# Kernel tuning notes

Hardware: AMD Instinct MI355X
Metric: run time of the kernel (lower is better)

Reference implementation:

```python
import jax, jax.numpy as jnp
import numpy as np

DIVERSITY_WEIGHT = 0.3
UNCERTAINTY_WEIGHT = 0.3
EPS_NORM = 1e-12  # torch F.normalize eps
EPS_LOG = 1e-8


def setup_inputs() -> dict:
    key = jax.random.key(0)
    k1, k2 = jax.random.split(key)
    B, N, D, C = 8, 8192, 512, 2
    x = jax.random.normal(k1, (B, N, D), dtype=jnp.float32)
    c = jax.random.normal(k2, (B, N, C), dtype=jnp.float32)
    return {"x": x, "c": c, "big_lambda": 512}


def reference(x, c, big_lambda):
    B, N, D = x.shape
    C = c.shape[-1]
    big_lambda = min(big_lambda, N)

    # relevance: max class score per instance (C > 1 branch)
    if C == 1:
        relevance = c[..., 0]
    else:
        relevance = jnp.max(c, axis=-1)  # [B, N]

    # diversity: 1 - mean cosine similarity to all other patches.
    # Row-sum of the N x N cosine-sim matrix factorizes:
    #   sum_j xn_i . xn_j = xn_i . (sum_j xn_j)  -> O(N*D) instead of O(N^2*D)
    norms = jnp.linalg.norm(x, axis=-1, keepdims=True)
    x_norm = x / jnp.maximum(norms, EPS_NORM)          # [B, N, D]
    s = jnp.sum(x_norm, axis=1)                        # [B, D]
    row_sums = jnp.einsum('bnd,bd->bn', x_norm, s)     # [B, N]
    avg_sim = (row_sums - 1.0) / (N - 1)
    diversity = 1.0 - avg_sim

    # uncertainty: entropy of class distribution
    if C == 1:
        p = jax.nn.sigmoid(c[..., 0])
        probs = jnp.stack([1.0 - p, p], axis=-1)
    else:
        probs = jax.nn.softmax(c, axis=-1)
    uncertainty = -jnp.sum(probs * jnp.log(probs + EPS_LOG), axis=-1)  # [B, N]

    combined = relevance + DIVERSITY_WEIGHT * diversity + UNCERTAINTY_WEIGHT * uncertainty

    _, selected_indices = jax.lax.top_k(combined, big_lambda)  # [B, big_lambda]
    attention_weights = jax.nn.softmax(combined, axis=1)       # [B, N]
    return selected_indices, attention_weights
```

## Files before the change

kernel.cpp:

```cpp
#include <hip/hip_runtime.h>
#include <stdint.h>

#define B 8
#define N 8192
#define D 512
#define K 512
#define DIV_W 0.3f
#define UNC_W 0.3f

constexpr int ROWS_PER_WAVE  = 16;
constexpr int WAVES_PER_BLK  = 4;
constexpr int ROWS_PER_BLOCK = ROWS_PER_WAVE * WAVES_PER_BLK;
constexpr int BLOCKS_PER_B   = N / ROWS_PER_BLOCK;

constexpr float DIVC = DIV_W * (1.0f + 1.0f / 8191.0f);
constexpr float COEF = DIV_W / 8191.0f;

__device__ __forceinline__ uint32_t ordmap(float f) {
    uint32_t u = __float_as_uint(f);
    return (u & 0x80000000u) ? ~u : (u | 0x80000000u);
}
__device__ __forceinline__ float ordunmap(uint32_t u) {
    return (u >> 31) ? __uint_as_float(u & 0x7FFFFFFFu) : __uint_as_float(~u);
}

__global__ __launch_bounds__(256) void k_norm_s(const float* __restrict__ x,
                                                const float* __restrict__ c,
                                                float* __restrict__ inv_norm,
                                                float* __restrict__ partials,
                                                float* __restrict__ combined) {
    int blk  = blockIdx.x;
    int b    = blk / BLOCKS_PER_B;
    int rb   = (blk % BLOCKS_PER_B) * ROWS_PER_BLOCK;
    int tid  = threadIdx.x;
    int wave = tid >> 6;
    int lane = tid & 63;

    const float4* xb = (const float4*)(x + (size_t)b * N * D);

    float4 accA = {0.f, 0.f, 0.f, 0.f};
    float4 accB = {0.f, 0.f, 0.f, 0.f};

    int row0 = rb + wave * ROWS_PER_WAVE;
    for (int r = 0; r < ROWS_PER_WAVE; ++r) {
        int row = row0 + r;
        const float4* xr = xb + (size_t)row * (D / 4);
        float4 a  = xr[lane];
        float4 bb = xr[64 + lane];

        float ss = a.x*a.x + a.y*a.y + a.z*a.z + a.w*a.w
                 + bb.x*bb.x + bb.y*bb.y + bb.z*bb.z + bb.w*bb.w;
        #pragma unroll
        for (int o = 32; o > 0; o >>= 1) ss += __shfl_xor(ss, o, 64);

        float inv = 1.0f / fmaxf(sqrtf(ss), 1e-12f);
        if (lane == 0) inv_norm[b * N + row] = inv;

        accA.x += a.x * inv;  accA.y += a.y * inv;
        accA.z += a.z * inv;  accA.w += a.w * inv;
        accB.x += bb.x * inv; accB.y += bb.y * inv;
        accB.z += bb.z * inv; accB.w += bb.w * inv;
    }

    if (lane < 16) {
        int row = row0 + lane;
        float2 cv = ((const float2*)(c))[(size_t)b * N + row];
        float rel = fmaxf(cv.x, cv.y);
        float e0 = expf(cv.x - rel), e1 = expf(cv.y - rel);
        float Z  = e0 + e1;
        float p0 = e0 / Z, p1 = e1 / Z;
        float ent = -(p0 * logf(p0 + 1e-8f) + p1 * logf(p1 + 1e-8f));
        combined[b * N + row] = rel + UNC_W * ent + DIVC;
    }

    __shared__ float sp[WAVES_PER_BLK][D];
    float* dA = &sp[wave][lane * 4];
    dA[0] = accA.x; dA[1] = accA.y; dA[2] = accA.z; dA[3] = accA.w;
    float* dB = &sp[wave][256 + lane * 4];
    dB[0] = accB.x; dB[1] = accB.y; dB[2] = accB.z; dB[3] = accB.w;
    __syncthreads();

    float* dst = partials + (size_t)blk * D;
    for (int d = tid; d < D; d += 256)
        dst[d] = sp[0][d] + sp[1][d] + sp[2][d] + sp[3][d];
}

__global__ __launch_bounds__(512) void k_reduce_s(const float* __restrict__ partials,
                                                  float* __restrict__ s) {
    int b = blockIdx.x;
    int d = threadIdx.x;
    const float* p = partials + (size_t)b * BLOCKS_PER_B * D + d;
    float acc = 0.f;
    #pragma unroll 16
    for (int j = 0; j < BLOCKS_PER_B; ++j) acc += p[(size_t)j * D];
    s[b * D + d] = acc;
}

__global__ __launch_bounds__(256) void k_combined(const float* __restrict__ x,
                                                  const float* __restrict__ inv_norm,
                                                  const float* __restrict__ s,
                                                  float* __restrict__ combined) {
    __shared__ float sl[D];
    int blk  = blockIdx.x;
    int b    = blk / BLOCKS_PER_B;
    int rb   = (blk % BLOCKS_PER_B) * ROWS_PER_BLOCK;
    int tid  = threadIdx.x;
    int wave = tid >> 6;
    int lane = tid & 63;

    for (int d = tid; d < D; d += 256) sl[d] = s[b * D + d];
    __syncthreads();

    const float4* sv = (const float4*)sl;
    float4 sA = sv[lane];
    float4 sB = sv[64 + lane];

    const float4* xb = (const float4*)(x + (size_t)b * N * D);
    int row0 = rb + wave * ROWS_PER_WAVE;
    for (int r = 0; r < ROWS_PER_WAVE; ++r) {
        int row = row0 + r;
        const float4* xr = xb + (size_t)row * (D / 4);
        float4 a  = xr[lane];
        float4 bb = xr[64 + lane];

        float dot = a.x*sA.x + a.y*sA.y + a.z*sA.z + a.w*sA.w
                  + bb.x*sB.x + bb.y*sB.y + bb.z*sB.z + bb.w*sB.w;
        #pragma unroll
        for (int o = 32; o > 0; o >>= 1) dot += __shfl_xor(dot, o, 64);

        if (lane == 0) {
            float rs = dot * inv_norm[b * N + row];
            combined[b * N + row] = combined[b * N + row] - COEF * rs;
        }
    }
}

__global__ __launch_bounds__(1024) void k_topk_sm(const float* __restrict__ combined,
                                                  float* __restrict__ out_idx,
                                                  float* __restrict__ out_w) {
    __shared__ uint64_t cand[K];
    __shared__ uint32_t hist[256];
    __shared__ uint32_t tiew[256];
    __shared__ uint32_t wred[16];
    __shared__ float    fred[16];
    __shared__ uint32_t sc_prefix, sc_remK, sc_cnt;

    const int b    = blockIdx.x;
    const int tid  = threadIdx.x;
    const int lane = tid & 63;
    const int wave = tid >> 6;

    const float4* cb4 = (const float4*)(combined + b * N);
    float4 f0 = cb4[tid];
    float4 f1 = cb4[1024 + tid];

    uint32_t v[8];
    v[0] = ordmap(f0.x); v[1] = ordmap(f0.y); v[2] = ordmap(f0.z); v[3] = ordmap(f0.w);
    v[4] = ordmap(f1.x); v[5] = ordmap(f1.y); v[6] = ordmap(f1.z); v[7] = ordmap(f1.w);

    uint32_t umax = 0;
    #pragma unroll
    for (int q = 0; q < 8; ++q) umax = max(umax, v[q]);
    #pragma unroll
    for (int o = 32; o > 0; o >>= 1) umax = max(umax, __shfl_xor(umax, o, 64));
    if (lane == 0) wred[wave] = umax;
    if (tid == 0) { sc_remK = K; sc_prefix = 0u; sc_cnt = 0u; }
    __syncthreads();
    uint32_t bmax = wred[0];
    #pragma unroll
    for (int q = 1; q < 16; ++q) bmax = max(bmax, wred[q]);
    const float m = ordunmap(bmax);

    float e[8];
    float sum = 0.f;
    #pragma unroll
    for (int q = 0; q < 8; ++q) { e[q] = expf(ordunmap(v[q]) - m); sum += e[q]; }
    #pragma unroll
    for (int o = 32; o > 0; o >>= 1) sum += __shfl_xor(sum, o, 64);
    if (lane == 0) fred[wave] = sum;
    __syncthreads();
    float Z = 0.f;
    #pragma unroll
    for (int q = 0; q < 16; ++q) Z += fred[q];
    const float invZ = 1.0f / Z;
    float4* ow = (float4*)(out_w + b * N);
    float4 w0 = {e[0]*invZ, e[1]*invZ, e[2]*invZ, e[3]*invZ};
    float4 w1 = {e[4]*invZ, e[5]*invZ, e[6]*invZ, e[7]*invZ};
    ow[tid]        = w0;
    ow[1024 + tid] = w1;

    uint32_t prefix = 0, maskHi = 0;
    for (int p = 3; p >= 0; --p) {
        if (tid < 256) hist[tid] = 0u;
        __syncthreads();
        const int sh = 8 * p;
        if (p == 3) {
            #pragma unroll
            for (int q = 0; q < 8; ++q) {
                uint32_t bin = v[q] >> 24;
                bool pred = true;
                unsigned long long todo = ~0ULL;
                while (todo) {
                    int leader = __ffsll(todo) - 1;
                    uint32_t lbin = __shfl(bin, leader, 64);
                    unsigned long long same = __ballot(pred && (bin == lbin));
                    if (lane == leader) atomicAdd(&hist[lbin], (uint32_t)__popcll(same));
                    todo &= ~same;
                    if (bin == lbin) pred = false;
                }
            }
        } else {
            #pragma unroll
            for (int q = 0; q < 8; ++q) {
                if ((v[q] & maskHi) == prefix)
                    atomicAdd(&hist[(v[q] >> sh) & 0xFFu], 1u);
            }
        }
        __syncthreads();
        if (wave == 0) {
            uint32_t cc[4], lsum = 0;
            #pragma unroll
            for (int q = 0; q < 4; ++q) { cc[q] = hist[lane * 4 + q]; lsum += cc[q]; }
            uint32_t ssum = lsum;
            #pragma unroll
            for (int off = 1; off < 64; off <<= 1) {
                uint32_t t2 = __shfl_down(ssum, off, 64);
                if (lane + off < 64) ssum += t2;
            }
            uint32_t cum = ssum - lsum;
            const uint32_t remK = sc_remK;
            #pragma unroll
            for (int q = 3; q >= 0; --q) {
                if (cum < remK && cum + cc[q] >= remK) {
                    sc_prefix = prefix | ((uint32_t)(lane * 4 + q) << sh);
                    sc_remK   = remK - cum;
                }
                cum += cc[q];
            }
        }
        __syncthreads();
        prefix = sc_prefix;
        maskHi |= (0xFFu << sh);
    }
    const uint32_t T    = prefix;
    const uint32_t remF = sc_remK;

    if (tid < 256) tiew[tid] = 0u;
    __syncthreads();
    #pragma unroll
    for (int q = 0; q < 8; ++q) {
        uint32_t idx = (q < 4) ? (uint32_t)(4 * tid + q)
                               : (uint32_t)(4096 + 4 * tid + (q - 4));
        bool g = (v[q] > T);
        unsigned long long mask = __ballot(g);
        if (mask) {
            int leader = __ffsll(mask) - 1;
            uint32_t bcnt = (uint32_t)__popcll(mask);
            uint32_t wbase = 0;
            if (lane == leader) wbase = atomicAdd(&sc_cnt, bcnt);
            wbase = __shfl(wbase, leader, 64);
            if (g) {
                uint32_t off = (uint32_t)__popcll(mask & ((1ULL << lane) - 1ULL));
                cand[wbase + off] = ((uint64_t)v[q] << 13) | (uint32_t)(8191 - idx);
            }
        }
        if (v[q] == T) atomicOr(&tiew[idx >> 5], 1u << (idx & 31));
    }
    __syncthreads();
    const uint32_t base = sc_cnt;
    if (wave == 0) {
        const int w0i = lane * 4;
        uint32_t lsum = 0;
        #pragma unroll
        for (int q = 0; q < 4; ++q) lsum += __popc(tiew[w0i + q]);
        uint32_t ssum = lsum;
        #pragma unroll
        for (int off = 1; off < 64; off <<= 1) {
            uint32_t t2 = __shfl_up(ssum, off, 64);
            if (lane >= off) ssum += t2;
        }
        uint32_t rank = ssum - lsum;
        for (int q = 0; q < 4; ++q) {
            uint32_t word = tiew[w0i + q];
            while (word) {
                int bpos = __builtin_ctz(word);
                if (rank < remF) {
                    uint32_t idx = (uint32_t)(w0i + q) * 32u + (uint32_t)bpos;
                    cand[base + rank] = ((uint64_t)T << 13) | (uint32_t)(8191 - idx);
                }
                rank++;
                word &= word - 1;
            }
        }
    }
    __syncthreads();

    uint64_t sv = (tid < K) ? cand[tid] : 0ULL;
    __syncthreads();
    for (int k = 2; k <= K; k <<= 1) {
        for (int j = k >> 1; j > 0; j >>= 1) {
            const bool desc  = ((tid & k) == 0);
            const bool lower = ((tid & j) == 0);
            uint64_t pv;
            if (j >= 64) {
                if (tid < K) cand[tid] = sv;
                __syncthreads();
                pv = (tid < K) ? cand[tid ^ j] : 0ULL;
                __syncthreads();
            } else {
                pv = __shfl_xor(sv, j, 64);
            }
            const bool keepmax = (lower == desc);
            if (tid < K && (keepmax ? (pv > sv) : (pv < sv))) sv = pv;
        }
    }
    if (tid < K)
        out_idx[b * K + tid] = (float)(8191u - (uint32_t)(sv & 0x1FFFu));
}

extern "C" void kernel_launch(void* const* d_in, const int* in_sizes, int n_in,
                              void* d_out, int out_size, void* d_ws, size_t ws_size,
                              hipStream_t stream) {
    const float* x = (const float*)d_in[0];
    const float* c = (const float*)d_in[1];

    float* ws       = (float*)d_ws;
    float* partials = ws;
    float* s        = partials + B * BLOCKS_PER_B * D;
    float* inv_norm = s + B * D;
    float* combined = inv_norm + B * N;

    float* out = (float*)d_out;

    k_norm_s  <<<B * BLOCKS_PER_B, 256, 0, stream>>>(x, c, inv_norm, partials, combined);
    k_reduce_s<<<B, 512, 0, stream>>>(partials, s);
    k_combined<<<B * BLOCKS_PER_B, 256, 0, stream>>>(x, inv_norm, s, combined);
    k_topk_sm <<<B, 1024, 0, stream>>>(combined, out, out + B * K);
}
```

Baseline: 81.14 us.

## Fuse all stages into one persistent kernel with software grid barriers

Replaces the four kernel launches with a single persistent kernel of 256 blocks × 512 threads that runs the norm and partial-sum pass, the per-batch reduction, the dot-product pass and the top-k/softmax pass, separated by atomic-based grid barriers. It also enlarges the per-block work from 64 to 256 rows and has the top-k stage use 512 threads holding 16 values each. The aim is to remove launch gaps and per-kernel ramp-up. The cost is barrier spin latency, a hipMemsetAsync on every call, and a reliance on all 256 blocks being co-resident, which can deadlock if they are not. Only 8 blocks do the reduction and top-k work while the rest sit idle.

New measurement: 172.3 us. +112.3%, slower.

```diff
diff --git a/kernel.cpp b/kernel.cpp
--- a/kernel.cpp
+++ b/kernel.cpp
@@ -8,10 +8,11 @@
 #define DIV_W 0.3f
 #define UNC_W 0.3f
 
-constexpr int ROWS_PER_WAVE  = 16;
-constexpr int WAVES_PER_BLK  = 4;
-constexpr int ROWS_PER_BLOCK = ROWS_PER_WAVE * WAVES_PER_BLK;
-constexpr int BLOCKS_PER_B   = N / ROWS_PER_BLOCK;
+constexpr int GRID    = 256;
+constexpr int THREADS = 512;
+constexpr int WAVES   = 8;
+constexpr int BLOCKS_PER_BATCH = 32;
+constexpr int ROWS_PER_BLOCK   = 256;
 
 constexpr float DIVC = DIV_W * (1.0f + 1.0f / 8191.0f);
 constexpr float COEF = DIV_W / 8191.0f;
@@ -24,298 +25,314 @@
     return (u >> 31) ? __uint_as_float(u & 0x7FFFFFFFu) : __uint_as_float(~u);
 }
 
-__global__ __launch_bounds__(256) void k_norm_s(const float* __restrict__ x,
-                                                const float* __restrict__ c,
-                                                float* __restrict__ inv_norm,
-                                                float* __restrict__ partials,
-                                                float* __restrict__ combined) {
-    int blk  = blockIdx.x;
-    int b    = blk / BLOCKS_PER_B;
-    int rb   = (blk % BLOCKS_PER_B) * ROWS_PER_BLOCK;
-    int tid  = threadIdx.x;
-    int wave = tid >> 6;
-    int lane = tid & 63;
-
+__device__ __forceinline__ void grid_barrier(unsigned int* bar) {
+    __syncthreads();
+    if (threadIdx.x == 0) {
+        __threadfence();
+        unsigned int g = atomicAdd(&bar[1], 0u);
+        __threadfence();
+        unsigned int prev = atomicAdd(&bar[0], 1u);
+        if (prev == GRID - 1) {
+            atomicExch(&bar[0], 0u);
+            __threadfence();
+            atomicAdd(&bar[1], 1u);
+        } else {
+            while (atomicAdd(&bar[1], 0u) == g)
+                __builtin_amdgcn_s_sleep(8);
+        }
+        __threadfence();
+    }
+    __syncthreads();
+}
+
+struct P3 {
+    unsigned long long cand[K];
+    uint32_t hist[256];
+    uint32_t tiew[256];
+    uint32_t wred[WAVES];
+    float    fred[WAVES];
+    uint32_t sc_prefix, sc_remK, sc_cnt;
+};
+
+__global__ __launch_bounds__(THREADS, 2) void k_fused(
+    const float* __restrict__ x, const float* __restrict__ c,
+    float* __restrict__ inv_norm, float* __restrict__ partials,
+    float* __restrict__ s, float* __restrict__ combined,
+    float* __restrict__ out_idx, float* __restrict__ out_w,
+    unsigned int* __restrict__ bar)
+{
+    __shared__ __align__(16) unsigned char smem[WAVES * D * 4];
+    float (*sp)[D] = (float(*)[D])smem;
+
+    const int bid  = blockIdx.x;
+    const int tid  = threadIdx.x;
+    const int wave = tid >> 6;
+    const int lane = tid & 63;
+
+    const int b     = bid >> 5;
+    const int rbase = (bid & 31) * ROWS_PER_BLOCK;
     const float4* xb = (const float4*)(x + (size_t)b * N * D);
 
-    float4 accA = {0.f, 0.f, 0.f, 0.f};
-    float4 accB = {0.f, 0.f, 0.f, 0.f};
-
-    int row0 = rb + wave * ROWS_PER_WAVE;
-    for (int r = 0; r < ROWS_PER_WAVE; ++r) {
-        int row = row0 + r;
-        const float4* xr = xb + (size_t)row * (D / 4);
-        float4 a  = xr[lane];
-        float4 bb = xr[64 + lane];
-
-        float ss = a.x*a.x + a.y*a.y + a.z*a.z + a.w*a.w
-                 + bb.x*bb.x + bb.y*bb.y + bb.z*bb.z + bb.w*bb.w;
-        #pragma unroll
-        for (int o = 32; o > 0; o >>= 1) ss += __shfl_xor(ss, o, 64);
-
-        float inv = 1.0f / fmaxf(sqrtf(ss), 1e-12f);
-        if (lane == 0) inv_norm[b * N + row] = inv;
-
-        accA.x += a.x * inv;  accA.y += a.y * inv;
-        accA.z += a.z * inv;  accA.w += a.w * inv;
-        accB.x += bb.x * inv; accB.y += bb.y * inv;
-        accB.z += bb.z * inv; accB.w += bb.w * inv;
-    }
-
-    if (lane < 16) {
-        int row = row0 + lane;
-        float2 cv = ((const float2*)(c))[(size_t)b * N + row];
-        float rel = fmaxf(cv.x, cv.y);
-        float e0 = expf(cv.x - rel), e1 = expf(cv.y - rel);
-        float Z  = e0 + e1;
-        float p0 = e0 / Z, p1 = e1 / Z;
-        float ent = -(p0 * logf(p0 + 1e-8f) + p1 * logf(p1 + 1e-8f));
-        combined[b * N + row] = rel + UNC_W * ent + DIVC;
-    }
-
-    __shared__ float sp[WAVES_PER_BLK][D];
-    float* dA = &sp[wave][lane * 4];
-    dA[0] = accA.x; dA[1] = accA.y; dA[2] = accA.z; dA[3] = accA.w;
-    float* dB = &sp[wave][256 + lane * 4];
-    dB[0] = accB.x; dB[1] = accB.y; dB[2] = accB.z; dB[3] = accB.w;
-    __syncthreads();
-
-    float* dst = partials + (size_t)blk * D;
-    for (int d = tid; d < D; d += 256)
-        dst[d] = sp[0][d] + sp[1][d] + sp[2][d] + sp[3][d];
-}
-
-__global__ __launch_bounds__(512) void k_reduce_s(const float* __restrict__ partials,
-                                                  float* __restrict__ s) {
-    int b = blockIdx.x;
-    int d = threadIdx.x;
-    const float* p = partials + (size_t)b * BLOCKS_PER_B * D + d;
-    float acc = 0.f;
-    #pragma unroll 16
-    for (int j = 0; j < BLOCKS_PER_B; ++j) acc += p[(size_t)j * D];
-    s[b * D + d] = acc;
-}
-
-__global__ __launch_bounds__(256) void k_combined(const float* __restrict__ x,
-                                                  const float* __restrict__ inv_norm,
-                                                  const float* __restrict__ s,
-                                                  float* __restrict__ combined) {
-    __shared__ float sl[D];
-    int blk  = blockIdx.x;
-    int b    = blk / BLOCKS_PER_B;
-    int rb   = (blk % BLOCKS_PER_B) * ROWS_PER_BLOCK;
-    int tid  = threadIdx.x;
-    int wave = tid >> 6;
-    int lane = tid & 63;
-
-    for (int d = tid; d < D; d += 256) sl[d] = s[b * D + d];
-    __syncthreads();
-
-    const float4* sv = (const float4*)sl;
-    float4 sA = sv[lane];
-    float4 sB = sv[64 + lane];
-
-    const float4* xb = (const float4*)(x + (size_t)b * N * D);
-    int row0 = rb + wave * ROWS_PER_WAVE;
-    for (int r = 0; r < ROWS_PER_WAVE; ++r) {
-        int row = row0 + r;
-        const float4* xr = xb + (size_t)row * (D / 4);
-        float4 a  = xr[lane];
-        float4 bb = xr[64 + lane];
-
-        float dot = a.x*sA.x + a.y*sA.y + a.z*sA.z + a.w*sA.w
-                  + bb.x*sB.x + bb.y*sB.y + bb.z*sB.z + bb.w*sB.w;
-        #pragma unroll
-        for (int o = 32; o > 0; o >>= 1) dot += __shfl_xor(dot, o, 64);
-
-        if (lane == 0) {
-            float rs = dot * inv_norm[b * N + row];
-            combined[b * N + row] = combined[b * N + row] - COEF * rs;
-        }
-    }
-}
-
-__global__ __launch_bounds__(1024) void k_topk_sm(const float* __restrict__ combined,
-                                                  float* __restrict__ out_idx,
-                                                  float* __restrict__ out_w) {
-    __shared__ uint64_t cand[K];
-    __shared__ uint32_t hist[256];
-    __shared__ uint32_t tiew[256];
-    __shared__ uint32_t wred[16];
-    __shared__ float    fred[16];
-    __shared__ uint32_t sc_prefix, sc_remK, sc_cnt;
-
-    const int b    = blockIdx.x;
-    const int tid  = threadIdx.x;
-    const int lane = tid & 63;
-    const int wave = tid >> 6;
-
-    const float4* cb4 = (const float4*)(combined + b * N);
-    float4 f0 = cb4[tid];
-    float4 f1 = cb4[1024 + tid];
-
-    uint32_t v[8];
-    v[0] = ordmap(f0.x); v[1] = ordmap(f0.y); v[2] = ordmap(f0.z); v[3] = ordmap(f0.w);
-    v[4] = ordmap(f1.x); v[5] = ordmap(f1.y); v[6] = ordmap(f1.z); v[7] = ordmap(f1.w);
-
-    uint32_t umax = 0;
-    #pragma unroll
-    for (int q = 0; q < 8; ++q) umax = max(umax, v[q]);
-    #pragma unroll
-    for (int o = 32; o > 0; o >>= 1) umax = max(umax, __shfl_xor(umax, o, 64));
-    if (lane == 0) wred[wave] = umax;
-    if (tid == 0) { sc_remK = K; sc_prefix = 0u; sc_cnt = 0u; }
-    __syncthreads();
-    uint32_t bmax = wred[0];
-    #pragma unroll
-    for (int q = 1; q < 16; ++q) bmax = max(bmax, wred[q]);
-    const float m = ordunmap(bmax);
-
-    float e[8];
-    float sum = 0.f;
-    #pragma unroll
-    for (int q = 0; q < 8; ++q) { e[q] = expf(ordunmap(v[q]) - m); sum += e[q]; }
-    #pragma unroll
-    for (int o = 32; o > 0; o >>= 1) sum += __shfl_xor(sum, o, 64);
-    if (lane == 0) fred[wave] = sum;
-    __syncthreads();
-    float Z = 0.f;
-    #pragma unroll
-    for (int q = 0; q < 16; ++q) Z += fred[q];
-    const float invZ = 1.0f / Z;
-    float4* ow = (float4*)(out_w + b * N);
-    float4 w0 = {e[0]*invZ, e[1]*invZ, e[2]*invZ, e[3]*invZ};
-    float4 w1 = {e[4]*invZ, e[5]*invZ, e[6]*invZ, e[7]*invZ};
-    ow[tid]        = w0;
-    ow[1024 + tid] = w1;
-
-    uint32_t prefix = 0, maskHi = 0;
-    for (int p = 3; p >= 0; --p) {
-        if (tid < 256) hist[tid] = 0u;
-        __syncthreads();
-        const int sh = 8 * p;
-        if (p == 3) {
+    {
+        float4 accA = {0.f,0.f,0.f,0.f}, accB = {0.f,0.f,0.f,0.f};
+        #pragma unroll
+        for (int chunk = 0; chunk < 2; ++chunk) {
+            const int row0 = rbase + chunk * 128 + wave * 16;
+            #pragma unroll 4
+            for (int r = 0; r < 16; ++r) {
+                const int row = row0 + r;
+                const float4* xr = xb + (size_t)row * (D / 4);
+                float4 a  = xr[lane];
+                float4 bb = xr[64 + lane];
+
+                float ss = a.x*a.x + a.y*a.y + a.z*a.z + a.w*a.w
+                         + bb.x*bb.x + bb.y*bb.y + bb.z*bb.z + bb.w*bb.w;
+                #pragma unroll
+                for (int o = 32; o > 0; o >>= 1) ss += __shfl_xor(ss, o, 64);
+
+                float inv = 1.0f / fmaxf(sqrtf(ss), 1e-12f);
+                if (lane == 0) inv_norm[b * N + row] = inv;
+
+                accA.x += a.x * inv;  accA.y += a.y * inv;
+                accA.z += a.z * inv;  accA.w += a.w * inv;
+                accB.x += bb.x * inv; accB.y += bb.y * inv;
+                accB.z += bb.z * inv; accB.w += bb.w * inv;
+            }
+            if (lane < 16) {
+                const int row = row0 + lane;
+                float2 cv = ((const float2*)c)[(size_t)b * N + row];
+                float rel = fmaxf(cv.x, cv.y);
+                float e0 = expf(cv.x - rel), e1 = expf(cv.y - rel);
+                float Z  = e0 + e1;
+                float p0 = e0 / Z, p1 = e1 / Z;
+                float ent = -(p0 * logf(p0 + 1e-8f) + p1 * logf(p1 + 1e-8f));
+                combined[b * N + row] = rel + UNC_W * ent + DIVC;
+            }
+        }
+
+        float* dA = &sp[wave][lane * 4];
+        dA[0] = accA.x; dA[1] = accA.y; dA[2] = accA.z; dA[3] = accA.w;
+        float* dB = &sp[wave][256 + lane * 4];
+        dB[0] = accB.x; dB[1] = accB.y; dB[2] = accB.z; dB[3] = accB.w;
+        __syncthreads();
+
+        float v = 0.f;
+        #pragma unroll
+        for (int w = 0; w < WAVES; ++w) v += sp[w][tid];
+        partials[(size_t)bid * D + tid] = v;
+    }
+    grid_barrier(bar);
+
+    if (bid < B) {
+        const float* p = partials + (size_t)bid * BLOCKS_PER_BATCH * D + tid;
+        float acc = 0.f;
+        #pragma unroll 8
+        for (int j = 0; j < BLOCKS_PER_BATCH; ++j) acc += p[(size_t)j * D];
+        s[bid * D + tid] = acc;
+    }
+    grid_barrier(bar);
+
+    {
+        float* sl = (float*)smem;
+        sl[tid] = s[b * D + tid];
+        __syncthreads();
+        float4 sA = ((const float4*)sl)[lane];
+        float4 sB = ((const float4*)sl)[64 + lane];
+
+        #pragma unroll
+        for (int chunk = 0; chunk < 2; ++chunk) {
+            const int row0 = rbase + chunk * 128 + wave * 16;
+            #pragma unroll 4
+            for (int r = 0; r < 16; ++r) {
+                const int row = row0 + r;
+                const float4* xr = xb + (size_t)row * (D / 4);
+                float4 a  = xr[lane];
+                float4 bb = xr[64 + lane];
+
+                float dot = a.x*sA.x + a.y*sA.y + a.z*sA.z + a.w*sA.w
+                          + bb.x*sB.x + bb.y*sB.y + bb.z*sB.z + bb.w*sB.w;
+                #pragma unroll
+                for (int o = 32; o > 0; o >>= 1) dot += __shfl_xor(dot, o, 64);
+
+                if (lane == 0) {
+                    float rs = dot * inv_norm[b * N + row];
+                    combined[b * N + row] -= COEF * rs;
+                }
+            }
+        }
+    }
+    grid_barrier(bar);
+
+    if (bid >= B) return;
+    {
+        P3* p3 = (P3*)smem;
+        const int bb3 = bid;
+        const float4* cb4 = (const float4*)(combined + bb3 * N);
+
+        uint32_t v[16];
+        uint32_t umax = 0;
+        #pragma unroll
+        for (int g = 0; g < 4; ++g) {
+            float4 f = cb4[tid + 512 * g];
+            v[4*g+0] = ordmap(f.x); v[4*g+1] = ordmap(f.y);
+            v[4*g+2] = ordmap(f.z); v[4*g+3] = ordmap(f.w);
+            umax = max(umax, max(max(v[4*g+0], v[4*g+1]), max(v[4*g+2], v[4*g+3])));
+        }
+        #pragma unroll
+        for (int o = 32; o > 0; o >>= 1) umax = max(umax, __shfl_xor(umax, o, 64));
+        if (lane == 0) p3->wred[wave] = umax;
+        if (tid == 0) { p3->sc_remK = K; p3->sc_prefix = 0u; p3->sc_cnt = 0u; }
+        __syncthreads();
+        uint32_t bmax = p3->wred[0];
+        #pragma unroll
+        for (int q = 1; q < WAVES; ++q) bmax = max(bmax, p3->wred[q]);
+        const float m = ordunmap(bmax);
+
+        float e[16];
+        float sum = 0.f;
+        #pragma unroll
+        for (int q = 0; q < 16; ++q) { e[q] = expf(ordunmap(v[q]) - m); sum += e[q]; }
+        #pragma unroll
+        for (int o = 32; o > 0; o >>= 1) sum += __shfl_xor(sum, o, 64);
+        if (lane == 0) p3->fred[wave] = sum;
+        __syncthreads();
+        float Z = 0.f;
+        #pragma unroll
+        for (int q = 0; q < WAVES; ++q) Z += p3->fred[q];
+        const float invZ = 1.0f / Z;
+        float4* ow = (float4*)(out_w + bb3 * N);
+        #pragma unroll
+        for (int g = 0; g < 4; ++g) {
+            float4 w = {e[4*g+0]*invZ, e[4*g+1]*invZ, e[4*g+2]*invZ, e[4*g+3]*invZ};
+            ow[tid + 512 * g] = w;
+        }
+
+        uint32_t prefix = 0, maskHi = 0;
+        for (int p = 3; p >= 0; --p) {
+            if (tid < 256) p3->hist[tid] = 0u;
+            __syncthreads();
+            const int sh = 8 * p;
+            if (p == 3) {
+                #pragma unroll
+                for (int q = 0; q < 16; ++q) {
+                    uint32_t bin = v[q] >> 24;
+                    bool pred = true;
+                    unsigned long long todo = ~0ULL;
+                    while (todo) {
+                        int leader = __ffsll(todo) - 1;
+                        uint32_t lbin = __shfl(bin, leader, 64);
+                        unsigned long long same = __ballot(pred && (bin == lbin));
+                        if (lane == leader) atomicAdd(&p3->hist[lbin], (uint32_t)__popcll(same));
+                        todo &= ~same;
+                        if (bin == lbin) pred = false;
+                    }
+                }
+            } else {
+                #pragma unroll
+                for (int q = 0; q < 16; ++q) {
+                    if ((v[q] & maskHi) == prefix)
+                        atomicAdd(&p3->hist[(v[q] >> sh) & 0xFFu], 1u);
+                }
+            }
+            __syncthreads();
+            if (wave == 0) {
+                uint32_t cc[4], lsum = 0;
+                #pragma unroll
+                for (int q = 0; q < 4; ++q) { cc[q] = p3->hist[lane * 4 + q]; lsum += cc[q]; }
+                uint32_t ssum = lsum;
+                #pragma unroll
+                for (int off = 1; off < 64; off <<= 1) {
+                    uint32_t t2 = __shfl_down(ssum, off, 64);
+                    if (lane + off < 64) ssum += t2;
+                }
+                uint32_t cum = ssum - lsum;
+                const uint32_t remK = p3->sc_remK;
+                #pragma unroll
+                for (int q = 3; q >= 0; --q) {
+                    if (cum < remK && cum + cc[q] >= remK) {
+                        p3->sc_prefix = prefix | ((uint32_t)(lane * 4 + q) << sh);
+                        p3->sc_remK   = remK - cum;
+                    }
+                    cum += cc[q];
+                }
+            }
+            __syncthreads();
+            prefix = p3->sc_prefix;
+            maskHi |= (0xFFu << sh);
+        }
+        const uint32_t T    = prefix;
+        const uint32_t remF = p3->sc_remK;
+
+        if (tid < 256) p3->tiew[tid] = 0u;
+        __syncthreads();
+        #pragma unroll
+        for (int q = 0; q < 16; ++q) {
+            uint32_t idx = 4u * tid + 2048u * (q >> 2) + (q & 3);
+            bool g = (v[q] > T);
+            unsigned long long mask = __ballot(g);
+            if (mask) {
+                int leader = __ffsll(mask) - 1;
+                uint32_t bcnt = (uint32_t)__popcll(mask);
+                uint32_t wbase = 0;
+                if (lane == leader) wbase = atomicAdd(&p3->sc_cnt, bcnt);
+                wbase = __shfl(wbase, leader, 64);
+                if (g) {
+                    uint32_t off = (uint32_t)__popcll(mask & ((1ULL << lane) - 1ULL));
+                    p3->cand[wbase + off] = ((uint64_t)v[q] << 13) | (uint32_t)(8191 - idx);
+                }
+            }
+            if (v[q] == T) atomicOr(&p3->tiew[idx >> 5], 1u << (idx & 31));
+        }
+        __syncthreads();
+        const uint32_t base = p3->sc_cnt;
+        if (wave == 0) {
+            const int w0i = lane * 4;
+            uint32_t lsum = 0;
             #pragma unroll
-            for (int q = 0; q < 8; ++q) {
-                uint32_t bin = v[q] >> 24;
-                bool pred = true;
-                unsigned long long todo = ~0ULL;
-                while (todo) {
-                    int leader = __ffsll(todo) - 1;
-                    uint32_t lbin = __shfl(bin, leader, 64);
-                    unsigned long long same = __ballot(pred && (bin == lbin));
-                    if (lane == leader) atomicAdd(&hist[lbin], (uint32_t)__popcll(same));
-                    todo &= ~same;
-                    if (bin == lbin) pred = false;
-                }
-            }
-        } else {
-            #pragma unroll
-            for (int q = 0; q < 8; ++q) {
-                if ((v[q] & maskHi) == prefix)
-                    atomicAdd(&hist[(v[q] >> sh) & 0xFFu], 1u);
-            }
-        }
-        __syncthreads();
-        if (wave == 0) {
-            uint32_t cc[4], lsum = 0;
-            #pragma unroll
-            for (int q = 0; q < 4; ++q) { cc[q] = hist[lane * 4 + q]; lsum += cc[q]; }
+            for (int q = 0; q < 4; ++q) lsum += __popc(p3->tiew[w0i + q]);
             uint32_t ssum = lsum;
             #pragma unroll
             for (int off = 1; off < 64; off <<= 1) {
-                uint32_t t2 = __shfl_down(ssum, off, 64);
-                if (lane + off < 64) ssum += t2;
-            }
-            uint32_t cum = ssum - lsum;
-            const uint32_t remK = sc_remK;
-            #pragma unroll
-            for (int q = 3; q >= 0; --q) {
-                if (cum < remK && cum + cc[q] >= remK) {
-                    sc_prefix = prefix | ((uint32_t)(lane * 4 + q) << sh);
-                    sc_remK   = remK - cum;
-                }
-                cum += cc[q];
-            }
-        }
-        __syncthreads();
-        prefix = sc_prefix;
-        maskHi |= (0xFFu << sh);
-    }
-    const uint32_t T    = prefix;
-    const uint32_t remF = sc_remK;
-
-    if (tid < 256) tiew[tid] = 0u;
-    __syncthreads();
-    #pragma unroll
-    for (int q = 0; q < 8; ++q) {
-        uint32_t idx = (q < 4) ? (uint32_t)(4 * tid + q)
-                               : (uint32_t)(4096 + 4 * tid + (q - 4));
-        bool g = (v[q] > T);
-        unsigned long long mask = __ballot(g);
-        if (mask) {
-            int leader = __ffsll(mask) - 1;
-            uint32_t bcnt = (uint32_t)__popcll(mask);
-            uint32_t wbase = 0;
-            if (lane == leader) wbase = atomicAdd(&sc_cnt, bcnt);
-            wbase = __shfl(wbase, leader, 64);
-            if (g) {
-                uint32_t off = (uint32_t)__popcll(mask & ((1ULL << lane) - 1ULL));
-                cand[wbase + off] = ((uint64_t)v[q] << 13) | (uint32_t)(8191 - idx);
-            }
-        }
-        if (v[q] == T) atomicOr(&tiew[idx >> 5], 1u << (idx & 31));
-    }
-    __syncthreads();
-    const uint32_t base = sc_cnt;
-    if (wave == 0) {
-        const int w0i = lane * 4;
-        uint32_t lsum = 0;
-        #pragma unroll
-        for (int q = 0; q < 4; ++q) lsum += __popc(tiew[w0i + q]);
-        uint32_t ssum = lsum;
-        #pragma unroll
-        for (int off = 1; off < 64; off <<= 1) {
-            uint32_t t2 = __shfl_up(ssum, off, 64);
-            if (lane >= off) ssum += t2;
-        }
-        uint32_t rank = ssum - lsum;
-        for (int q = 0; q < 4; ++q) {
-            uint32_t word = tiew[w0i + q];
-            while (word) {
-                int bpos = __builtin_ctz(word);
-                if (rank < remF) {
-                    uint32_t idx = (uint32_t)(w0i + q) * 32u + (uint32_t)bpos;
-                    cand[base + rank] = ((uint64_t)T << 13) | (uint32_t)(8191 - idx);
-                }
-                rank++;
-                word &= word - 1;
-            }
-        }
-    }
-    __syncthreads();
-
-    uint64_t sv = (tid < K) ? cand[tid] : 0ULL;
-    __syncthreads();
-    for (int k = 2; k <= K; k <<= 1) {
-        for (int j = k >> 1; j > 0; j >>= 1) {
-            const bool desc  = ((tid & k) == 0);
-            const bool lower = ((tid & j) == 0);
-            uint64_t pv;
-            if (j >= 64) {
-                if (tid < K) cand[tid] = sv;
-                __syncthreads();
-                pv = (tid < K) ? cand[tid ^ j] : 0ULL;
-                __syncthreads();
-            } else {
-                pv = __shfl_xor(sv, j, 64);
-            }
-            const bool keepmax = (lower == desc);
-            if (tid < K && (keepmax ? (pv > sv) : (pv < sv))) sv = pv;
-        }
-    }
-    if (tid < K)
-        out_idx[b * K + tid] = (float)(8191u - (uint32_t)(sv & 0x1FFFu));
+                uint32_t t2 = __shfl_up(ssum, off, 64);
+                if (lane >= off) ssum += t2;
+            }
+            uint32_t rank = ssum - lsum;
+            for (int q = 0; q < 4; ++q) {
+                uint32_t word = p3->tiew[w0i + q];
+                while (word) {
+                    int bpos = __builtin_ctz(word);
+                    if (rank < remF) {
+                        uint32_t idx = (uint32_t)(w0i + q) * 32u + (uint32_t)bpos;
+                        p3->cand[base + rank] = ((uint64_t)T << 13) | (uint32_t)(8191 - idx);
+                    }
+                    rank++;
+                    word &= word - 1;
+                }
+            }
+        }
+        __syncthreads();
+
+        uint64_t sv = p3->cand[tid];
+        __syncthreads();
+        for (int k = 2; k <= K; k <<= 1) {
+            for (int j = k >> 1; j > 0; j >>= 1) {
+                const bool desc  = ((tid & k) == 0);
+                const bool lower = ((tid & j) == 0);
+                uint64_t pv;
+                if (j >= 64) {
+                    p3->cand[tid] = sv;
+                    __syncthreads();
+                    pv = p3->cand[tid ^ j];
+                    __syncthreads();
+                } else {
+                    pv = __shfl_xor(sv, j, 64);
+                }
+                const bool keepmax = (lower == desc);
+                if (keepmax ? (pv > sv) : (pv < sv)) sv = pv;
+            }
+        }
+        out_idx[bb3 * K + tid] = (float)(8191u - (uint32_t)(sv & 0x1FFFu));
+    }
 }
 
 extern "C" void kernel_launch(void* const* d_in, const int* in_sizes, int n_in,
@@ -324,16 +341,17 @@
     const float* x = (const float*)d_in[0];
     const float* c = (const float*)d_in[1];
 
-    float* ws       = (float*)d_ws;
-    float* partials = ws;
-    float* s        = partials + B * BLOCKS_PER_B * D;
+    unsigned int* bar = (unsigned int*)d_ws;
+    float* base     = (float*)d_ws + 16;
+    float* partials = base;
+    float* s        = partials + GRID * D;
     float* inv_norm = s + B * D;
     float* combined = inv_norm + B * N;
 
-    float* out = (float*)d_out;
-
-    k_norm_s  <<<B * BLOCKS_PER_B, 256, 0, stream>>>(x, c, inv_norm, partials, combined);
-    k_reduce_s<<<B, 512, 0, stream>>>(partials, s);
-    k_combined<<<B * BLOCKS_PER_B, 256, 0, stream>>>(x, inv_norm, s, combined);
-    k_topk_sm <<<B, 1024, 0, stream>>>(combined, out, out + B * K);
-}
+    float* out_idx = (float*)d_out;
+    float* out_w   = out_idx + B * K;
+
+    hipMemsetAsync(bar, 0, 64, stream);
+    k_fused<<<GRID, THREADS, 0, stream>>>(x, c, inv_norm, partials, s, combined,
+                                          out_idx, out_w, bar);
+}
```

## Replace bitonic sort of top-k candidates with parallel rank-by-counting

Applied to the files above, without the earlier changes.

The final ordering of the 512 selected candidates swaps the bitonic sorting network, which needed many shared-memory exchanges and block barriers, for a rank count. Each of 1024 threads counts how many keys in half of the candidate list exceed its own key, the two partial ranks are summed, and each index is scattered to its rank. This cuts the barrier count to one, at the cost of O(K^2) shared-memory comparisons. Unroll pragmas are also added to the row loops of the norm and dot kernels.

Result: no change. 81.31 us (+0.2%).

```diff
diff --git a/kernel.cpp b/kernel.cpp
--- a/kernel.cpp
+++ b/kernel.cpp
@@ -42,6 +42,7 @@
     float4 accB = {0.f, 0.f, 0.f, 0.f};
 
     int row0 = rb + wave * ROWS_PER_WAVE;
+    #pragma unroll 4
     for (int r = 0; r < ROWS_PER_WAVE; ++r) {
         int row = row0 + r;
         const float4* xr = xb + (size_t)row * (D / 4);
@@ -64,7 +65,7 @@
 
     if (lane < 16) {
         int row = row0 + lane;
-        float2 cv = ((const float2*)(c))[(size_t)b * N + row];
+        float2 cv = ((const float2*)c)[(size_t)b * N + row];
         float rel = fmaxf(cv.x, cv.y);
         float e0 = expf(cv.x - rel), e1 = expf(cv.y - rel);
         float Z  = e0 + e1;
@@ -117,6 +118,7 @@
 
     const float4* xb = (const float4*)(x + (size_t)b * N * D);
     int row0 = rb + wave * ROWS_PER_WAVE;
+    #pragma unroll 4
     for (int r = 0; r < ROWS_PER_WAVE; ++r) {
         int row = row0 + r;
         const float4* xr = xb + (size_t)row * (D / 4);
@@ -130,20 +132,25 @@
 
         if (lane == 0) {
             float rs = dot * inv_norm[b * N + row];
-            combined[b * N + row] = combined[b * N + row] - COEF * rs;
-        }
-    }
-}
+            combined[b * N + row] -= COEF * rs;
+        }
+    }
+}
+
+struct P3 {
+    unsigned long long cand[K];
+    uint32_t hist[256];
+    uint32_t tiew[256];
+    uint16_t rnk[2][K];
+    uint32_t wred[16];
+    float    fred[16];
+    uint32_t sc_prefix, sc_remK, sc_cnt;
+};
 
 __global__ __launch_bounds__(1024) void k_topk_sm(const float* __restrict__ combined,
                                                   float* __restrict__ out_idx,
                                                   float* __restrict__ out_w) {
-    __shared__ uint64_t cand[K];
-    __shared__ uint32_t hist[256];
-    __shared__ uint32_t tiew[256];
-    __shared__ uint32_t wred[16];
-    __shared__ float    fred[16];
-    __shared__ uint32_t sc_prefix, sc_remK, sc_cnt;
+    __shared__ P3 p3;
 
     const int b    = blockIdx.x;
     const int tid  = threadIdx.x;
@@ -163,12 +170,12 @@
     for (int q = 0; q < 8; ++q) umax = max(umax, v[q]);
     #pragma unroll
     for (int o = 32; o > 0; o >>= 1) umax = max(umax, __shfl_xor(umax, o, 64));
-    if (lane == 0) wred[wave] = umax;
-    if (tid == 0) { sc_remK = K; sc_prefix = 0u; sc_cnt = 0u; }
-    __syncthreads();
-    uint32_t bmax = wred[0];
-    #pragma unroll
-    for (int q = 1; q < 16; ++q) bmax = max(bmax, wred[q]);
+    if (lane == 0) p3.wred[wave] = umax;
+    if (tid == 0) { p3.sc_remK = K; p3.sc_prefix = 0u; p3.sc_cnt = 0u; }
+    __syncthreads();
+    uint32_t bmax = p3.wred[0];
+    #pragma unroll
+    for (int q = 1; q < 16; ++q) bmax = max(bmax, p3.wred[q]);
     const float m = ordunmap(bmax);
 
     float e[8];
@@ -177,11 +184,11 @@
     for (int q = 0; q < 8; ++q) { e[q] = expf(ordunmap(v[q]) - m); sum += e[q]; }
     #pragma unroll
     for (int o = 32; o > 0; o >>= 1) sum += __shfl_xor(sum, o, 64);
-    if (lane == 0) fred[wave] = sum;
+    if (lane == 0) p3.fred[wave] = sum;
     __syncthreads();
     float Z = 0.f;
     #pragma unroll
-    for (int q = 0; q < 16; ++q) Z += fred[q];
+    for (int q = 0; q < 16; ++q) Z += p3.fred[q];
     const float invZ = 1.0f / Z;
     float4* ow = (float4*)(out_w + b * N);
     float4 w0 = {e[0]*invZ, e[1]*invZ, e[2]*invZ, e[3]*invZ};
@@ -191,7 +198,7 @@
 
     uint32_t prefix = 0, maskHi = 0;
     for (int p = 3; p >= 0; --p) {
-        if (tid < 256) hist[tid] = 0u;
+        if (tid < 256) p3.hist[tid] = 0u;
         __syncthreads();
         const int sh = 8 * p;
         if (p == 3) {
@@ -204,7 +211,7 @@
                     int leader = __ffsll(todo) - 1;
                     uint32_t lbin = __shfl(bin, leader, 64);
                     unsigned long long same = __ballot(pred && (bin == lbin));
-                    if (lane == leader) atomicAdd(&hist[lbin], (uint32_t)__popcll(same));
+                    if (lane == leader) atomicAdd(&p3.hist[lbin], (uint32_t)__popcll(same));
                     todo &= ~same;
                     if (bin == lbin) pred = false;
                 }
@@ -213,14 +220,14 @@
             #pragma unroll
             for (int q = 0; q < 8; ++q) {
                 if ((v[q] & maskHi) == prefix)
-                    atomicAdd(&hist[(v[q] >> sh) & 0xFFu], 1u);
+                    atomicAdd(&p3.hist[(v[q] >> sh) & 0xFFu], 1u);
             }
         }
         __syncthreads();
         if (wave == 0) {
             uint32_t cc[4], lsum = 0;
             #pragma unroll
-            for (int q = 0; q < 4; ++q) { cc[q] = hist[lane * 4 + q]; lsum += cc[q]; }
+            for (int q = 0; q < 4; ++q) { cc[q] = p3.hist[lane * 4 + q]; lsum += cc[q]; }
             uint32_t ssum = lsum;
             #pragma unroll
             for (int off = 1; off < 64; off <<= 1) {
@@ -228,24 +235,24 @@
                 if (lane + off < 64) ssum += t2;
             }
             uint32_t cum = ssum - lsum;
-            const uint32_t remK = sc_remK;
+            const uint32_t remK = p3.sc_remK;
             #pragma unroll
             for (int q = 3; q >= 0; --q) {
                 if (cum < remK && cum + cc[q] >= remK) {
-                    sc_prefix = prefix | ((uint32_t)(lane * 4 + q) << sh);
-                    sc_remK   = remK - cum;
+                    p3.sc_prefix = prefix | ((uint32_t)(lane * 4 + q) << sh);
+                    p3.sc_remK   = remK - cum;
                 }
                 cum += cc[q];
             }
         }
         __syncthreads();
-        prefix = sc_prefix;
+        prefix = p3.sc_prefix;
         maskHi |= (0xFFu << sh);
     }
     const uint32_t T    = prefix;
-    const uint32_t remF = sc_remK;
-
-    if (tid < 256) tiew[tid] = 0u;
+    const uint32_t remF = p3.sc_remK;
+
+    if (tid < 256) p3.tiew[tid] = 0u;
     __syncthreads();
     #pragma unroll
     for (int q = 0; q < 8; ++q) {
@@ -257,22 +264,22 @@
             int leader = __ffsll(mask) - 1;
             uint32_t bcnt = (uint32_t)__popcll(mask);
             uint32_t wbase = 0;
-            if (lane == leader) wbase = atomicAdd(&sc_cnt, bcnt);
+            if (lane == leader) wbase = atomicAdd(&p3.sc_cnt, bcnt);
             wbase = __shfl(wbase, leader, 64);
             if (g) {
                 uint32_t off = (uint32_t)__popcll(mask & ((1ULL << lane) - 1ULL));
-                cand[wbase + off] = ((uint64_t)v[q] << 13) | (uint32_t)(8191 - idx);
-            }
-        }
-        if (v[q] == T) atomicOr(&tiew[idx >> 5], 1u << (idx & 31));
-    }
-    __syncthreads();
-    const uint32_t base = sc_cnt;
+                p3.cand[wbase + off] = ((uint64_t)v[q] << 13) | (uint32_t)(8191 - idx);
+            }
+        }
+        if (v[q] == T) atomicOr(&p3.tiew[idx >> 5], 1u << (idx & 31));
+    }
+    __syncthreads();
+    const uint32_t base = p3.sc_cnt;
     if (wave == 0) {
         const int w0i = lane * 4;
         uint32_t lsum = 0;
         #pragma unroll
-        for (int q = 0; q < 4; ++q) lsum += __popc(tiew[w0i + q]);
+        for (int q = 0; q < 4; ++q) lsum += __popc(p3.tiew[w0i + q]);
         uint32_t ssum = lsum;
         #pragma unroll
         for (int off = 1; off < 64; off <<= 1) {
@@ -281,12 +288,12 @@
         }
         uint32_t rank = ssum - lsum;
         for (int q = 0; q < 4; ++q) {
-            uint32_t word = tiew[w0i + q];
+            uint32_t word = p3.tiew[w0i + q];
             while (word) {
                 int bpos = __builtin_ctz(word);
                 if (rank < remF) {
                     uint32_t idx = (uint32_t)(w0i + q) * 32u + (uint32_t)bpos;
-                    cand[base + rank] = ((uint64_t)T << 13) | (uint32_t)(8191 - idx);
+                    p3.cand[base + rank] = ((uint64_t)T << 13) | (uint32_t)(8191 - idx);
                 }
                 rank++;
                 word &= word - 1;
@@ -295,27 +302,23 @@
     }
     __syncthreads();
 
-    uint64_t sv = (tid < K) ? cand[tid] : 0ULL;
-    __syncthreads();
-    for (int k = 2; k <= K; k <<= 1) {
-        for (int j = k >> 1; j > 0; j >>= 1) {
-            const bool desc  = ((tid & k) == 0);
-            const bool lower = ((tid & j) == 0);
-            uint64_t pv;
-            if (j >= 64) {
-                if (tid < K) cand[tid] = sv;
-                __syncthreads();
-                pv = (tid < K) ? cand[tid ^ j] : 0ULL;
-                __syncthreads();
-            } else {
-                pv = __shfl_xor(sv, j, 64);
-            }
-            const bool keepmax = (lower == desc);
-            if (tid < K && (keepmax ? (pv > sv) : (pv < sv))) sv = pv;
-        }
-    }
-    if (tid < K)
-        out_idx[b * K + tid] = (float)(8191u - (uint32_t)(sv & 0x1FFFu));
+    {
+        const int ki   = tid & 511;
+        const int half = tid >> 9;
+        const uint64_t me = p3.cand[ki];
+        const int j0 = half * 256;
+        uint32_t cnt = 0;
+        #pragma unroll 8
+        for (int j = 0; j < 256; ++j)
+            cnt += (p3.cand[j0 + j] > me) ? 1u : 0u;
+        p3.rnk[half][ki] = (uint16_t)cnt;
+    }
+    __syncthreads();
+    if (tid < K) {
+        uint32_t rank = (uint32_t)p3.rnk[0][tid] + (uint32_t)p3.rnk[1][tid];
+        uint32_t idx  = 8191u - (uint32_t)(p3.cand[tid] & 0x1FFFu);
+        out_idx[b * K + rank] = (float)idx;
+    }
 }
 
 extern "C" void kernel_launch(void* const* d_in, const int* in_sizes, int n_in,
```
